# Kernel tuning notes

Measured on AMD Instinct MI355X. Metric: run time of the kernel, lower is better.

The kernel has to match this reference:

```python
import jax, jax.numpy as jnp
import numpy as np

N_NODES = 50000
N_EDGES = 640000
IN_F, H1, H2, H3, N_CLS = 128, 128, 128, 128, 40


def setup_inputs() -> dict:
    key = jax.random.key(0)
    ks = jax.random.split(key, 16)
    def lin(k, i, o):
        bound = 1.0 / np.sqrt(i)
        kw, kb = jax.random.split(k)
        W = jax.random.uniform(kw, (i, o), jnp.float32, -bound, bound)
        b = jax.random.uniform(kb, (o,), jnp.float32, -bound, bound)
        return W, b
    Wr, br = lin(ks[0], IN_F, H3)
    W1, b1 = lin(ks[1], IN_F, H1)
    W2, b2 = lin(ks[2], H1, H2)
    W3, b3 = lin(ks[3], H2, H3)
    Wop, bop = lin(ks[4], H3, N_CLS)
    x = jax.random.normal(ks[5], (N_NODES, IN_F), jnp.float32)
    src = jax.random.randint(ks[6], (N_EDGES,), 0, N_NODES, jnp.int64)
    dst = jax.random.randint(ks[7], (N_EDGES,), 0, N_NODES, jnp.int64)
    edge_weight = jax.random.uniform(ks[8], (N_EDGES,), jnp.float32)
    return {"x": x, "src": src, "dst": dst, "edge_weight": edge_weight,
            "Wr": Wr, "br": br, "W1": W1, "b1": b1, "W2": W2, "b2": b2,
            "W3": W3, "b3": b3, "Wop": Wop, "bop": bop}


def _gconv(x, src, dst, ew, W, b, n_nodes):
    # gather neighbor features, scale by edge weight, scatter-sum to dst, linear
    msg = x[src] * ew[:, None]                      # [E, d_in]
    agg = jax.ops.segment_sum(msg, dst, num_segments=n_nodes)  # [N, d_in]
    return agg @ W + b


def reference(x, src, dst, edge_weight, Wr, br, W1, b1, W2, b2, W3, b3, Wop, bop):
    n = x.shape[0]
    res = x @ Wr + br
    h = jax.nn.relu(_gconv(x, src, dst, edge_weight, W1, b1, n))
    h = jax.nn.relu(_gconv(h, src, dst, edge_weight, W2, b2, n))
    h = _gconv(h, src, dst, edge_weight, W3, b3, n)
    h = jax.nn.relu(h + res)
    return h @ Wop + bop
```

## Files before the change

### kernel.cpp

```cpp
#include <hip/hip_runtime.h>
#include <hip/hip_fp16.h>
#include <stdint.h>


#define NF 128

typedef unsigned short u16;
typedef unsigned int u32;
typedef __attribute__((ext_vector_type(8))) short short8;
typedef __attribute__((ext_vector_type(4))) float f32x4;

__device__ __forceinline__ float bf2f(u16 v) {
    union { unsigned u; float f; } x; x.u = (unsigned)v << 16; return x.f;
}
__device__ __forceinline__ u16 f2bf(float f) {
    union { float f; unsigned u; } x; x.f = f;
    unsigned r = (x.u + 0x7FFFu + ((x.u >> 16) & 1u)) >> 16;
    return (u16)r;
}

__global__ __launch_bounds__(256) void prep_all(
    const int* __restrict__ dst, int* __restrict__ counts, int* __restrict__ rank,
    int n_edges,
    const float* __restrict__ x, u16* __restrict__ xb, int n_feat,
    const float* __restrict__ Wr, const float* __restrict__ W1,
    const float* __restrict__ W2, const float* __restrict__ W3,
    const float* __restrict__ Wop, u16* __restrict__ Wt, u16* __restrict__ Wtop,
    int HB, int CB)
{
    int b = blockIdx.x;
    if (b < HB) {
        int e = b * 256 + threadIdx.x;
        if (e < n_edges) rank[e] = atomicAdd(&counts[dst[e]], 1);
    } else if (b < HB + CB) {
        int idx = ((b - HB) * 256 + threadIdx.x) * 4;
        if (idx < n_feat) {
            float4 v = *reinterpret_cast<const float4*>(x + idx);
            ushort4 o;
            o.x = f2bf(v.x); o.y = f2bf(v.y); o.z = f2bf(v.z); o.w = f2bf(v.w);
            *reinterpret_cast<ushort4*>(xb + idx) = o;
        }
    } else {
        int i = (b - HB - CB) * 256 + threadIdx.x;
        if (i < 4 * 16384) {
            int w = i >> 14, r = i & 16383;
            int nn = r >> 7, kk = r & 127;
            const float* W = (w == 0) ? Wr : (w == 1) ? W1 : (w == 2) ? W2 : W3;
            Wt[i] = f2bf(W[kk * NF + nn]);
        } else {
            int r = i - 4 * 16384;
            if (r < 48 * 128) {
                int nn = r >> 7, kk = r & 127;
                Wtop[r] = (nn < 40) ? f2bf(Wop[kk * 40 + nn]) : (u16)0;
            }
        }
    }
}

__global__ __launch_bounds__(256) void scan_pass1(
    const int* __restrict__ counts, int* __restrict__ bsums, int n)
{
    __shared__ int s[256];
    int i = blockIdx.x * 256 + threadIdx.x;
    int c = (i < n) ? counts[i] : 0;
    s[threadIdx.x] = (c + 3) & ~3;
    __syncthreads();
    for (int off = 128; off > 0; off >>= 1) {
        if (threadIdx.x < off) s[threadIdx.x] += s[threadIdx.x + off];
        __syncthreads();
    }
    if (threadIdx.x == 0) bsums[blockIdx.x] = s[0];
}

__global__ __launch_bounds__(256) void scan_pass23(
    int* __restrict__ rowptr, const int* __restrict__ bsums, int n, int G)
{
    __shared__ int s[256];
    int t = threadIdx.x;
    int bv = (t < G) ? bsums[t] : 0;
    s[t] = bv;
    __syncthreads();
    for (int off = 1; off < 256; off <<= 1) {
        int u = (t >= off) ? s[t - off] : 0;
        __syncthreads();
        s[t] += u;
        __syncthreads();
    }
    int blockoff = (blockIdx.x > 0) ? s[blockIdx.x - 1] : 0;
    int total = s[255];
    __syncthreads();

    int i = blockIdx.x * 256 + t;
    int c = (i < n) ? rowptr[i] : 0;
    int v = (c + 3) & ~3;
    s[t] = v;
    __syncthreads();
    for (int off = 1; off < 256; off <<= 1) {
        int u = (t >= off) ? s[t - off] : 0;
        __syncthreads();
        s[t] += u;
        __syncthreads();
    }
    int excl = s[t] - v + blockoff;
    if (i < n) rowptr[i] = excl;
    if (i == 0) rowptr[n] = total;
}

__global__ __launch_bounds__(256) void fill_packed(
    const int* __restrict__ src, const int* __restrict__ dst,
    const float* __restrict__ ew, const int* __restrict__ rowptr,
    const int* __restrict__ rank, u32* __restrict__ ppairs, int n_edges)
{
    int e = blockIdx.x * 256 + threadIdx.x;
    if (e >= n_edges) return;
    int pos = rowptr[dst[e]] + rank[e];
    ppairs[pos] = ((u32)src[e] << 16) |
                  (u32)__half_as_ushort(__float2half_rn(ew[e]));
}

__global__ __launch_bounds__(256) void agg_gather_b(
    const u16* __restrict__ xb, const int* __restrict__ rowptr,
    const u32* __restrict__ ppairs, u16* __restrict__ aggb, int n_nodes)
{
    int gid = blockIdx.x * 256 + threadIdx.x;
    int node = gid >> 4;
    if (node >= n_nodes) return;
    int f = (gid & 15) << 3;
    int e0 = rowptr[node];
    int e1 = rowptr[node + 1];
    const u16* xf = xb + f;

    float acc[8];
    #pragma unroll
    for (int j = 0; j < 8; j++) acc[j] = 0.f;

    int e = e0;
    for (; e + 8 <= e1; e += 8) {
        uint4 pa = *reinterpret_cast<const uint4*>(ppairs + e);
        uint4 pb = *reinterpret_cast<const uint4*>(ppairs + e + 4);
        u32 p[8] = {pa.x, pa.y, pa.z, pa.w, pb.x, pb.y, pb.z, pb.w};
        short8 v[8];
        #pragma unroll
        for (int k = 0; k < 8; k++)
            v[k] = *reinterpret_cast<const short8*>(xf + (size_t)(p[k] >> 16) * NF);
        #pragma unroll
        for (int k = 0; k < 8; k++) {
            float w = __half2float(__ushort_as_half((u16)(p[k] & 0xFFFFu)));
            #pragma unroll
            for (int j = 0; j < 8; j++)
                acc[j] = fmaf(bf2f((u16)v[k][j]), w, acc[j]);
        }
    }
    if (e < e1) {
        uint4 pa = *reinterpret_cast<const uint4*>(ppairs + e);
        u32 p[4] = {pa.x, pa.y, pa.z, pa.w};
        short8 v[4];
        #pragma unroll
        for (int k = 0; k < 4; k++)
            v[k] = *reinterpret_cast<const short8*>(xf + (size_t)(p[k] >> 16) * NF);
        #pragma unroll
        for (int k = 0; k < 4; k++) {
            float w = __half2float(__ushort_as_half((u16)(p[k] & 0xFFFFu)));
            #pragma unroll
            for (int j = 0; j < 8; j++)
                acc[j] = fmaf(bf2f((u16)v[k][j]), w, acc[j]);
        }
    }

    short8 o;
    #pragma unroll
    for (int j = 0; j < 8; j++) o[j] = (short)f2bf(acc[j]);
    *reinterpret_cast<short8*>(aggb + (size_t)node * NF + f) = o;
}

template<int RELU, int RES>
__global__ __launch_bounds__(256) void gemm_mfma128(
    const u16* __restrict__ A, const u16* __restrict__ Wt,
    const float* __restrict__ bias, const u16* __restrict__ resid,
    u16* __restrict__ out, int nrows)
{
    __shared__ u16 Bs[128 * 128];
    const int tid = threadIdx.x;
    #pragma unroll
    for (int i = 0; i < 8; i++) {
        int G = tid + i * 256;
        int row = G >> 4, g = G & 15, gs = g ^ (row & 7);
        *reinterpret_cast<short8*>(&Bs[row * NF + gs * 8]) =
            *reinterpret_cast<const short8*>(Wt + (size_t)G * 8);
    }
    __syncthreads();

    const int wave = tid >> 6, lane = tid & 63;
    const int lrow = lane & 15, lk = lane >> 4;

    #pragma unroll
    for (int sub = 0; sub < 2; ++sub) {
        const int row0 = blockIdx.x * 128 + sub * 64 + wave * 16;
        const int grow = row0 + lrow;

        short8 a[4];
        if (grow < nrows) {
            const u16* Ar = A + (size_t)grow * NF + lk * 8;
            #pragma unroll
            for (int t = 0; t < 4; t++)
                a[t] = *reinterpret_cast<const short8*>(Ar + t * 32);
        } else {
            #pragma unroll
            for (int t = 0; t < 4; t++)
                #pragma unroll
                for (int j = 0; j < 8; j++) a[t][j] = 0;
        }

        f32x4 acc[8];
        #pragma unroll
        for (int c = 0; c < 8; c++) { acc[c][0]=0.f; acc[c][1]=0.f; acc[c][2]=0.f; acc[c][3]=0.f; }

        #pragma unroll
        for (int t = 0; t < 4; t++) {
            #pragma unroll
            for (int c = 0; c < 8; c++) {
                int col = c * 16 + lrow;
                int g = t * 4 + lk, gs = g ^ (col & 7);
                short8 b = *reinterpret_cast<const short8*>(&Bs[col * NF + gs * 8]);
                acc[c] = __builtin_amdgcn_mfma_f32_16x16x32_bf16(a[t], b, acc[c], 0, 0, 0);
            }
        }

        #pragma unroll
        for (int c = 0; c < 8; c++) {
            int col = c * 16 + lrow;
            float bv = bias[col];
            #pragma unroll
            for (int r = 0; r < 4; r++) {
                int orow = row0 + lk * 4 + r;
                if (orow < nrows) {
                    float v = acc[c][r] + bv;
                    if (RES) v += bf2f(resid[(size_t)orow * NF + col]);
                    if (RELU) v = fmaxf(v, 0.f);
                    out[(size_t)orow * NF + col] = f2bf(v);
                }
            }
        }
    }
}

__global__ __launch_bounds__(256) void gemm_out40_mfma(
    const u16* __restrict__ H, const u16* __restrict__ Wtop,
    const float* __restrict__ bop, float* __restrict__ out, int nrows)
{
    __shared__ u16 Bs[48 * 128];
    const int tid = threadIdx.x;
    #pragma unroll
    for (int i = 0; i < 3; i++) {
        int G = tid + i * 256;
        int row = G >> 4, g = G & 15, gs = g ^ (row & 7);
        *reinterpret_cast<short8*>(&Bs[row * NF + gs * 8]) =
            *reinterpret_cast<const short8*>(Wtop + (size_t)G * 8);
    }
    __syncthreads();

    const int wave = tid >> 6, lane = tid & 63;
    const int lrow = lane & 15, lk = lane >> 4;

    #pragma unroll
    for (int sub = 0; sub < 2; ++sub) {
        const int row0 = blockIdx.x * 128 + sub * 64 + wave * 16;
        const int grow = row0 + lrow;

        short8 a[4];
        if (grow < nrows) {
            const u16* Hr = H + (size_t)grow * NF + lk * 8;
            #pragma unroll
            for (int t = 0; t < 4; t++)
                a[t] = *reinterpret_cast<const short8*>(Hr + t * 32);
        } else {
            #pragma unroll
            for (int t = 0; t < 4; t++)
                #pragma unroll
                for (int j = 0; j < 8; j++) a[t][j] = 0;
        }

        f32x4 acc[3];
        #pragma unroll
        for (int c = 0; c < 3; c++) { acc[c][0]=0.f; acc[c][1]=0.f; acc[c][2]=0.f; acc[c][3]=0.f; }

        #pragma unroll
        for (int t = 0; t < 4; t++) {
            #pragma unroll
            for (int c = 0; c < 3; c++) {
                int col = c * 16 + lrow;
                int g = t * 4 + lk, gs = g ^ (col & 7);
                short8 b = *reinterpret_cast<const short8*>(&Bs[col * NF + gs * 8]);
                acc[c] = __builtin_amdgcn_mfma_f32_16x16x32_bf16(a[t], b, acc[c], 0, 0, 0);
            }
        }

        #pragma unroll
        for (int c = 0; c < 3; c++) {
            int col = c * 16 + lrow;
            if (col < 40) {
                float bv = bop[col];
                #pragma unroll
                for (int r = 0; r < 4; r++) {
                    int orow = row0 + lk * 4 + r;
                    if (orow < nrows)
                        out[(size_t)orow * 40 + col] = acc[c][r] + bv;
                }
            }
        }
    }
}


extern "C" void kernel_launch(void* const* d_in, const int* in_sizes, int n_in,
                              void* d_out, int out_size, void* d_ws, size_t ws_size,
                              hipStream_t stream)
{
    const float* x   = (const float*)d_in[0];
    const int*   src = (const int*)d_in[1];
    const int*   dst = (const int*)d_in[2];
    const float* ew  = (const float*)d_in[3];
    const float* Wr  = (const float*)d_in[4];
    const float* br  = (const float*)d_in[5];
    const float* W1  = (const float*)d_in[6];
    const float* b1  = (const float*)d_in[7];
    const float* W2  = (const float*)d_in[8];
    const float* b2  = (const float*)d_in[9];
    const float* W3  = (const float*)d_in[10];
    const float* b3  = (const float*)d_in[11];
    const float* Wop = (const float*)d_in[12];
    const float* bop = (const float*)d_in[13];
    float* out = (float*)d_out;

    const int n_nodes = in_sizes[0] / NF;
    const int n_edges = in_sizes[1];
    const size_t feat = (size_t)n_nodes * NF;
    const int padded_cap = n_edges + 3 * n_nodes + 8;

    u16* xb   = (u16*)d_ws;
    u16* hb   = xb + feat;
    u16* aggb = hb + feat;
    u16* resb = aggb + feat;
    u16* Wt   = resb + feat;
    u16* Wtop = Wt + 4 * 16384;
    int* rowptr = (int*)(Wtop + 48 * 128);
    const int G1 = (n_nodes + 255) / 256;
    int* bsums  = rowptr + (n_nodes + 1);
    int* rank   = bsums + (G1 + 1);
    u32* ppairs = (u32*)(((uintptr_t)(rank + n_edges) + 15) & ~(uintptr_t)15);

    const int HB = (n_edges + 255) / 256;
    const int CB = ((int)feat / 4 + 255) / 256;
    const int PB = (4 * 16384 + 48 * 128 + 255) / 256;
    const int gemm_grid = (n_nodes + 127) / 128;
    const int agg_grid  = (n_nodes * 16 + 255) / 256;

    hipMemsetAsync(rowptr, 0, (size_t)(n_nodes + 1) * sizeof(int), stream);
    hipMemsetAsync(ppairs, 0, (size_t)padded_cap * sizeof(u32), stream);
    prep_all<<<HB + CB + PB, 256, 0, stream>>>(
        dst, rowptr, rank, n_edges, x, xb, (int)feat,
        Wr, W1, W2, W3, Wop, Wt, Wtop, HB, CB);
    scan_pass1<<<G1, 256, 0, stream>>>(rowptr, bsums, n_nodes);
    scan_pass23<<<G1, 256, 0, stream>>>(rowptr, bsums, n_nodes, G1);
    fill_packed<<<HB, 256, 0, stream>>>(src, dst, ew, rowptr, rank, ppairs, n_edges);

    gemm_mfma128<0, 0><<<gemm_grid, 256, 0, stream>>>(xb, Wt, br, nullptr, resb, n_nodes);

    agg_gather_b<<<agg_grid, 256, 0, stream>>>(xb, rowptr, ppairs, aggb, n_nodes);
    gemm_mfma128<1, 0><<<gemm_grid, 256, 0, stream>>>(aggb, Wt + 16384, b1, nullptr, hb, n_nodes);

    agg_gather_b<<<agg_grid, 256, 0, stream>>>(hb, rowptr, ppairs, aggb, n_nodes);
    gemm_mfma128<1, 0><<<gemm_grid, 256, 0, stream>>>(aggb, Wt + 2 * 16384, b2, nullptr, hb, n_nodes);

    agg_gather_b<<<agg_grid, 256, 0, stream>>>(hb, rowptr, ppairs, aggb, n_nodes);
    gemm_mfma128<1, 1><<<gemm_grid, 256, 0, stream>>>(aggb, Wt + 3 * 16384, b3, resb, hb, n_nodes);

    gemm_out40_mfma<<<gemm_grid, 256, 0, stream>>>(hb, Wtop, bop, out, n_nodes);
}
```

Before: 199.2 us.

## Fuse gather-aggregation with per-layer GEMM and final projection into one kernel

Each GNN layer now runs a single kernel: a block of 16 nodes gathers neighbor features into shared memory, then multiplies by the layer weight with MFMA and applies bias, ReLU and residual. The final layer also does the 40-class output projection in shared memory, so the aggb round trip and the separate output GEMM disappear. The residual GEMM is shrunk to 64 rows per block, and its A loads now overlap the weight staging. In exchange, weights are read straight from global/L2 with no LDS staging, and the 16-node blocks reload the weight matrix for every block.

```diff
diff --git a/kernel.cpp b/kernel.cpp
--- a/kernel.cpp
+++ b/kernel.cpp
@@ -118,66 +118,151 @@
                   (u32)__half_as_ushort(__float2half_rn(ew[e]));
 }
 
-__global__ __launch_bounds__(256) void agg_gather_b(
-    const u16* __restrict__ xb, const int* __restrict__ rowptr,
-    const u32* __restrict__ ppairs, u16* __restrict__ aggb, int n_nodes)
-{
-    int gid = blockIdx.x * 256 + threadIdx.x;
-    int node = gid >> 4;
-    if (node >= n_nodes) return;
-    int f = (gid & 15) << 3;
-    int e0 = rowptr[node];
-    int e1 = rowptr[node + 1];
-    const u16* xf = xb + f;
-
-    float acc[8];
-    #pragma unroll
-    for (int j = 0; j < 8; j++) acc[j] = 0.f;
-
-    int e = e0;
-    for (; e + 8 <= e1; e += 8) {
-        uint4 pa = *reinterpret_cast<const uint4*>(ppairs + e);
-        uint4 pb = *reinterpret_cast<const uint4*>(ppairs + e + 4);
-        u32 p[8] = {pa.x, pa.y, pa.z, pa.w, pb.x, pb.y, pb.z, pb.w};
-        short8 v[8];
-        #pragma unroll
-        for (int k = 0; k < 8; k++)
-            v[k] = *reinterpret_cast<const short8*>(xf + (size_t)(p[k] >> 16) * NF);
-        #pragma unroll
-        for (int k = 0; k < 8; k++) {
-            float w = __half2float(__ushort_as_half((u16)(p[k] & 0xFFFFu)));
+template<int RES, int PROJ>
+__global__ __launch_bounds__(256) void layer_gg(
+    const u16* __restrict__ X, const int* __restrict__ rowptr,
+    const u32* __restrict__ ppairs, const u16* __restrict__ Wt,
+    const float* __restrict__ bias, const u16* __restrict__ resid,
+    const u16* __restrict__ Wtop, const float* __restrict__ bop,
+    u16* __restrict__ hout, float* __restrict__ out, int n_nodes)
+{
+    __shared__ u16 As[16 * 128];
+    __shared__ u16 Hs[16 * 128];
+
+    const int tid = threadIdx.x;
+    const int node0 = blockIdx.x * 16;
+
+    {
+        const int nl = tid >> 4;
+        const int fl = tid & 15;
+        const int node = node0 + nl;
+        float acc[8];
+        #pragma unroll
+        for (int j = 0; j < 8; j++) acc[j] = 0.f;
+
+        if (node < n_nodes) {
+            const u16* xf = X + fl * 8;
+            int e0 = rowptr[node];
+            int e1 = rowptr[node + 1];
+            int e = e0;
+            for (; e + 8 <= e1; e += 8) {
+                uint4 pa = *reinterpret_cast<const uint4*>(ppairs + e);
+                uint4 pb = *reinterpret_cast<const uint4*>(ppairs + e + 4);
+                u32 p[8] = {pa.x, pa.y, pa.z, pa.w, pb.x, pb.y, pb.z, pb.w};
+                short8 v[8];
+                #pragma unroll
+                for (int k = 0; k < 8; k++)
+                    v[k] = *reinterpret_cast<const short8*>(xf + (size_t)(p[k] >> 16) * NF);
+                #pragma unroll
+                for (int k = 0; k < 8; k++) {
+                    float w = __half2float(__ushort_as_half((u16)(p[k] & 0xFFFFu)));
+                    #pragma unroll
+                    for (int j = 0; j < 8; j++)
+                        acc[j] = fmaf(bf2f((u16)v[k][j]), w, acc[j]);
+                }
+            }
+            if (e < e1) {
+                uint4 pa = *reinterpret_cast<const uint4*>(ppairs + e);
+                u32 p[4] = {pa.x, pa.y, pa.z, pa.w};
+                short8 v[4];
+                #pragma unroll
+                for (int k = 0; k < 4; k++)
+                    v[k] = *reinterpret_cast<const short8*>(xf + (size_t)(p[k] >> 16) * NF);
+                #pragma unroll
+                for (int k = 0; k < 4; k++) {
+                    float w = __half2float(__ushort_as_half((u16)(p[k] & 0xFFFFu)));
+                    #pragma unroll
+                    for (int j = 0; j < 8; j++)
+                        acc[j] = fmaf(bf2f((u16)v[k][j]), w, acc[j]);
+                }
+            }
+        }
+        short8 o;
+        #pragma unroll
+        for (int j = 0; j < 8; j++) o[j] = (short)f2bf(acc[j]);
+        int gs = fl ^ (nl & 7);
+        *reinterpret_cast<short8*>(&As[nl * NF + gs * 8]) = o;
+    }
+    __syncthreads();
+
+    const int wave = tid >> 6, lane = tid & 63;
+    const int lrow = lane & 15, lk = lane >> 4;
+
+    short8 a[4];
+    #pragma unroll
+    for (int t = 0; t < 4; t++) {
+        int g = t * 4 + lk, gs = g ^ (lrow & 7);
+        a[t] = *reinterpret_cast<const short8*>(&As[lrow * NF + gs * 8]);
+    }
+
+    f32x4 acc2[2];
+    #pragma unroll
+    for (int ct = 0; ct < 2; ct++) { acc2[ct][0]=0.f; acc2[ct][1]=0.f; acc2[ct][2]=0.f; acc2[ct][3]=0.f; }
+
+    #pragma unroll
+    for (int t = 0; t < 4; t++) {
+        #pragma unroll
+        for (int ct = 0; ct < 2; ct++) {
+            int col = wave * 32 + ct * 16 + lrow;
+            short8 b = *reinterpret_cast<const short8*>(Wt + (size_t)col * NF + (t * 4 + lk) * 8);
+            acc2[ct] = __builtin_amdgcn_mfma_f32_16x16x32_bf16(a[t], b, acc2[ct], 0, 0, 0);
+        }
+    }
+
+    #pragma unroll
+    for (int ct = 0; ct < 2; ct++) {
+        int col = wave * 32 + ct * 16 + lrow;
+        float bv = bias[col];
+        #pragma unroll
+        for (int r = 0; r < 4; r++) {
+            int row = lk * 4 + r;
+            int node = node0 + row;
+            if (node < n_nodes) {
+                float v = acc2[ct][r] + bv;
+                if (RES) v += bf2f(resid[(size_t)node * NF + col]);
+                v = fmaxf(v, 0.f);
+                if (!PROJ) {
+                    hout[(size_t)node * NF + col] = f2bf(v);
+                } else {
+                    Hs[row * NF + (((col >> 3) ^ (row & 7)) << 3) + (col & 7)] = f2bf(v);
+                }
+            }
+        }
+    }
+
+    if (PROJ) {
+        __syncthreads();
+        if (wave < 3) {
+            short8 pa[4];
             #pragma unroll
-            for (int j = 0; j < 8; j++)
-                acc[j] = fmaf(bf2f((u16)v[k][j]), w, acc[j]);
-        }
-    }
-    if (e < e1) {
-        uint4 pa = *reinterpret_cast<const uint4*>(ppairs + e);
-        u32 p[4] = {pa.x, pa.y, pa.z, pa.w};
-        short8 v[4];
-        #pragma unroll
-        for (int k = 0; k < 4; k++)
-            v[k] = *reinterpret_cast<const short8*>(xf + (size_t)(p[k] >> 16) * NF);
-        #pragma unroll
-        for (int k = 0; k < 4; k++) {
-            float w = __half2float(__ushort_as_half((u16)(p[k] & 0xFFFFu)));
+            for (int t = 0; t < 4; t++) {
+                int g = t * 4 + lk, gs = g ^ (lrow & 7);
+                pa[t] = *reinterpret_cast<const short8*>(&Hs[lrow * NF + gs * 8]);
+            }
+            f32x4 pacc;
+            pacc[0]=0.f; pacc[1]=0.f; pacc[2]=0.f; pacc[3]=0.f;
+            int col = wave * 16 + lrow;
             #pragma unroll
-            for (int j = 0; j < 8; j++)
-                acc[j] = fmaf(bf2f((u16)v[k][j]), w, acc[j]);
-        }
-    }
-
-    short8 o;
-    #pragma unroll
-    for (int j = 0; j < 8; j++) o[j] = (short)f2bf(acc[j]);
-    *reinterpret_cast<short8*>(aggb + (size_t)node * NF + f) = o;
-}
-
-template<int RELU, int RES>
-__global__ __launch_bounds__(256) void gemm_mfma128(
+            for (int t = 0; t < 4; t++) {
+                short8 b = *reinterpret_cast<const short8*>(Wtop + (size_t)col * NF + (t * 4 + lk) * 8);
+                pacc = __builtin_amdgcn_mfma_f32_16x16x32_bf16(pa[t], b, pacc, 0, 0, 0);
+            }
+            if (col < 40) {
+                float bv = bop[col];
+                #pragma unroll
+                for (int r = 0; r < 4; r++) {
+                    int node = node0 + lk * 4 + r;
+                    if (node < n_nodes)
+                        out[(size_t)node * 40 + col] = pacc[r] + bv;
+                }
+            }
+        }
+    }
+}
+
+__global__ __launch_bounds__(256) void gemm_mfma_res(
     const u16* __restrict__ A, const u16* __restrict__ Wt,
-    const float* __restrict__ bias, const u16* __restrict__ resid,
-    u16* __restrict__ out, int nrows)
+    const float* __restrict__ bias, u16* __restrict__ out, int nrows)
 {
     __shared__ u16 Bs[128 * 128];
     const int tid = threadIdx.x;
@@ -188,125 +273,50 @@
         *reinterpret_cast<short8*>(&Bs[row * NF + gs * 8]) =
             *reinterpret_cast<const short8*>(Wt + (size_t)G * 8);
     }
-    __syncthreads();
 
     const int wave = tid >> 6, lane = tid & 63;
     const int lrow = lane & 15, lk = lane >> 4;
-
-    #pragma unroll
-    for (int sub = 0; sub < 2; ++sub) {
-        const int row0 = blockIdx.x * 128 + sub * 64 + wave * 16;
-        const int grow = row0 + lrow;
-
-        short8 a[4];
-        if (grow < nrows) {
-            const u16* Ar = A + (size_t)grow * NF + lk * 8;
+    const int row0 = blockIdx.x * 64 + wave * 16;
+    const int grow = row0 + lrow;
+
+    short8 a[4];
+    if (grow < nrows) {
+        const u16* Ar = A + (size_t)grow * NF + lk * 8;
+        #pragma unroll
+        for (int t = 0; t < 4; t++)
+            a[t] = *reinterpret_cast<const short8*>(Ar + t * 32);
+    } else {
+        #pragma unroll
+        for (int t = 0; t < 4; t++)
             #pragma unroll
-            for (int t = 0; t < 4; t++)
-                a[t] = *reinterpret_cast<const short8*>(Ar + t * 32);
-        } else {
-            #pragma unroll
-            for (int t = 0; t < 4; t++)
-                #pragma unroll
-                for (int j = 0; j < 8; j++) a[t][j] = 0;
-        }
-
-        f32x4 acc[8];
-        #pragma unroll
-        for (int c = 0; c < 8; c++) { acc[c][0]=0.f; acc[c][1]=0.f; acc[c][2]=0.f; acc[c][3]=0.f; }
-
-        #pragma unroll
-        for (int t = 0; t < 4; t++) {
-            #pragma unroll
-            for (int c = 0; c < 8; c++) {
-                int col = c * 16 + lrow;
-                int g = t * 4 + lk, gs = g ^ (col & 7);
-                short8 b = *reinterpret_cast<const short8*>(&Bs[col * NF + gs * 8]);
-                acc[c] = __builtin_amdgcn_mfma_f32_16x16x32_bf16(a[t], b, acc[c], 0, 0, 0);
-            }
-        }
-
+            for (int j = 0; j < 8; j++) a[t][j] = 0;
+    }
+    __syncthreads();
+
+    f32x4 acc[8];
+    #pragma unroll
+    for (int c = 0; c < 8; c++) { acc[c][0]=0.f; acc[c][1]=0.f; acc[c][2]=0.f; acc[c][3]=0.f; }
+
+    #pragma unroll
+    for (int t = 0; t < 4; t++) {
         #pragma unroll
         for (int c = 0; c < 8; c++) {
             int col = c * 16 + lrow;
-            float bv = bias[col];
-            #pragma unroll
-            for (int r = 0; r < 4; r++) {
-                int orow = row0 + lk * 4 + r;
-                if (orow < nrows) {
-                    float v = acc[c][r] + bv;
-                    if (RES) v += bf2f(resid[(size_t)orow * NF + col]);
-                    if (RELU) v = fmaxf(v, 0.f);
-                    out[(size_t)orow * NF + col] = f2bf(v);
-                }
-            }
-        }
-    }
-}
-
-__global__ __launch_bounds__(256) void gemm_out40_mfma(
-    const u16* __restrict__ H, const u16* __restrict__ Wtop,
-    const float* __restrict__ bop, float* __restrict__ out, int nrows)
-{
-    __shared__ u16 Bs[48 * 128];
-    const int tid = threadIdx.x;
-    #pragma unroll
-    for (int i = 0; i < 3; i++) {
-        int G = tid + i * 256;
-        int row = G >> 4, g = G & 15, gs = g ^ (row & 7);
-        *reinterpret_cast<short8*>(&Bs[row * NF + gs * 8]) =
-            *reinterpret_cast<const short8*>(Wtop + (size_t)G * 8);
-    }
-    __syncthreads();
-
-    const int wave = tid >> 6, lane = tid & 63;
-    const int lrow = lane & 15, lk = lane >> 4;
-
-    #pragma unroll
-    for (int sub = 0; sub < 2; ++sub) {
-        const int row0 = blockIdx.x * 128 + sub * 64 + wave * 16;
-        const int grow = row0 + lrow;
-
-        short8 a[4];
-        if (grow < nrows) {
-            const u16* Hr = H + (size_t)grow * NF + lk * 8;
-            #pragma unroll
-            for (int t = 0; t < 4; t++)
-                a[t] = *reinterpret_cast<const short8*>(Hr + t * 32);
-        } else {
-            #pragma unroll
-            for (int t = 0; t < 4; t++)
-                #pragma unroll
-                for (int j = 0; j < 8; j++) a[t][j] = 0;
-        }
-
-        f32x4 acc[3];
-        #pragma unroll
-        for (int c = 0; c < 3; c++) { acc[c][0]=0.f; acc[c][1]=0.f; acc[c][2]=0.f; acc[c][3]=0.f; }
-
-        #pragma unroll
-        for (int t = 0; t < 4; t++) {
-            #pragma unroll
-            for (int c = 0; c < 3; c++) {
-                int col = c * 16 + lrow;
-                int g = t * 4 + lk, gs = g ^ (col & 7);
-                short8 b = *reinterpret_cast<const short8*>(&Bs[col * NF + gs * 8]);
-                acc[c] = __builtin_amdgcn_mfma_f32_16x16x32_bf16(a[t], b, acc[c], 0, 0, 0);
-            }
-        }
-
-        #pragma unroll
-        for (int c = 0; c < 3; c++) {
-            int col = c * 16 + lrow;
-            if (col < 40) {
-                float bv = bop[col];
-                #pragma unroll
-                for (int r = 0; r < 4; r++) {
-                    int orow = row0 + lk * 4 + r;
-                    if (orow < nrows)
-                        out[(size_t)orow * 40 + col] = acc[c][r] + bv;
-                }
-            }
+            int g = t * 4 + lk, gs = g ^ (col & 7);
+            short8 b = *reinterpret_cast<const short8*>(&Bs[col * NF + gs * 8]);
+            acc[c] = __builtin_amdgcn_mfma_f32_16x16x32_bf16(a[t], b, acc[c], 0, 0, 0);
+        }
+    }
+
+    #pragma unroll
+    for (int c = 0; c < 8; c++) {
+        int col = c * 16 + lrow;
+        float bv = bias[col];
+        #pragma unroll
+        for (int r = 0; r < 4; r++) {
+            int orow = row0 + lk * 4 + r;
+            if (orow < nrows)
+                out[(size_t)orow * NF + col] = f2bf(acc[c][r] + bv);
         }
     }
 }
@@ -338,9 +348,9 @@
     const int padded_cap = n_edges + 3 * n_nodes + 8;
 
     u16* xb   = (u16*)d_ws;
-    u16* hb   = xb + feat;
-    u16* aggb = hb + feat;
-    u16* resb = aggb + feat;
+    u16* h1b  = xb + feat;
+    u16* h2b  = h1b + feat;
+    u16* resb = h2b + feat;
     u16* Wt   = resb + feat;
     u16* Wtop = Wt + 4 * 16384;
     int* rowptr = (int*)(Wtop + 48 * 128);
@@ -352,8 +362,8 @@
     const int HB = (n_edges + 255) / 256;
     const int CB = ((int)feat / 4 + 255) / 256;
     const int PB = (4 * 16384 + 48 * 128 + 255) / 256;
-    const int gemm_grid = (n_nodes + 127) / 128;
-    const int agg_grid  = (n_nodes * 16 + 255) / 256;
+    const int res_grid   = (n_nodes + 63) / 64;
+    const int layer_grid = (n_nodes + 15) / 16;
 
     hipMemsetAsync(rowptr, 0, (size_t)(n_nodes + 1) * sizeof(int), stream);
     hipMemsetAsync(ppairs, 0, (size_t)padded_cap * sizeof(u32), stream);
@@ -364,16 +374,15 @@
     scan_pass23<<<G1, 256, 0, stream>>>(rowptr, bsums, n_nodes, G1);
     fill_packed<<<HB, 256, 0, stream>>>(src, dst, ew, rowptr, rank, ppairs, n_edges);
 
-    gemm_mfma128<0, 0><<<gemm_grid, 256, 0, stream>>>(xb, Wt, br, nullptr, resb, n_nodes);
-
-    agg_gather_b<<<agg_grid, 256, 0, stream>>>(xb, rowptr, ppairs, aggb, n_nodes);
-    gemm_mfma128<1, 0><<<gemm_grid, 256, 0, stream>>>(aggb, Wt + 16384, b1, nullptr, hb, n_nodes);
-
-    agg_gather_b<<<agg_grid, 256, 0, stream>>>(hb, rowptr, ppairs, aggb, n_nodes);
-    gemm_mfma128<1, 0><<<gemm_grid, 256, 0, stream>>>(aggb, Wt + 2 * 16384, b2, nullptr, hb, n_nodes);
-
-    agg_gather_b<<<agg_grid, 256, 0, stream>>>(hb, rowptr, ppairs, aggb, n_nodes);
-    gemm_mfma128<1, 1><<<gemm_grid, 256, 0, stream>>>(aggb, Wt + 3 * 16384, b3, resb, hb, n_nodes);
-
-    gemm_out40_mfma<<<gemm_grid, 256, 0, stream>>>(hb, Wtop, bop, out, n_nodes);
-}
+    gemm_mfma_res<<<res_grid, 256, 0, stream>>>(xb, Wt, br, resb, n_nodes);
+
+    layer_gg<0, 0><<<layer_grid, 256, 0, stream>>>(
+        xb, rowptr, ppairs, Wt + 16384, b1, nullptr, nullptr, nullptr,
+        h1b, nullptr, n_nodes);
+    layer_gg<0, 0><<<layer_grid, 256, 0, stream>>>(
+        h1b, rowptr, ppairs, Wt + 2 * 16384, b2, nullptr, nullptr, nullptr,
+        h2b, nullptr, n_nodes);
+    layer_gg<1, 1><<<layer_grid, 256, 0, stream>>>(
+        h2b, rowptr, ppairs, Wt + 3 * 16384, b3, resb, Wtop, bop,
+        nullptr, out, n_nodes);
+}
```

Result: faster. 191.1 us (-4.1%).

## Split gather into XCD-mapped feature slices and shrink GEMM row tiles

Applied to the files above, without the earlier changes.

The gather kernel now gives each block 64 nodes and one 32-feature slice. The slice is chosen from the block index modulo 8, so blocks running on the same pair of XCDs all touch the same quarter of the feature columns. That working set should fit in each XCD's L2 and reduce random-row misses to HBM. The mapping has 8 blocks per node group but only 4 slices, so every slice is computed and written twice, doubling gather compute and stores. Separately, the GEMM kernels now process 64 rows per block instead of 128, and issue the A-tile global loads before the barrier so they overlap with filling the weight tile in shared memory. This doubles the number of weight-tile loads.

```diff
diff --git a/kernel.cpp b/kernel.cpp
--- a/kernel.cpp
+++ b/kernel.cpp
@@ -118,18 +118,20 @@
                   (u32)__half_as_ushort(__float2half_rn(ew[e]));
 }
 
-__global__ __launch_bounds__(256) void agg_gather_b(
-    const u16* __restrict__ xb, const int* __restrict__ rowptr,
+__global__ __launch_bounds__(256) void gather_slice(
+    const u16* __restrict__ X, const int* __restrict__ rowptr,
     const u32* __restrict__ ppairs, u16* __restrict__ aggb, int n_nodes)
 {
-    int gid = blockIdx.x * 256 + threadIdx.x;
-    int node = gid >> 4;
+    const int b = blockIdx.x;
+    const int slice = (b & 7) >> 1;
+    const int t = threadIdx.x;
+    const int node = (b >> 3) * 64 + (t >> 2);
     if (node >= n_nodes) return;
-    int f = (gid & 15) << 3;
+    const int fo = slice * 32 + (t & 3) * 8;
+    const u16* xf = X + fo;
+
     int e0 = rowptr[node];
     int e1 = rowptr[node + 1];
-    const u16* xf = xb + f;
-
     float acc[8];
     #pragma unroll
     for (int j = 0; j < 8; j++) acc[j] = 0.f;
@@ -170,7 +172,7 @@
     short8 o;
     #pragma unroll
     for (int j = 0; j < 8; j++) o[j] = (short)f2bf(acc[j]);
-    *reinterpret_cast<short8*>(aggb + (size_t)node * NF + f) = o;
+    *reinterpret_cast<short8*>(aggb + (size_t)node * NF + fo) = o;
 }
 
 template<int RELU, int RES>
@@ -188,57 +190,53 @@
         *reinterpret_cast<short8*>(&Bs[row * NF + gs * 8]) =
             *reinterpret_cast<const short8*>(Wt + (size_t)G * 8);
     }
-    __syncthreads();
 
     const int wave = tid >> 6, lane = tid & 63;
     const int lrow = lane & 15, lk = lane >> 4;
-
-    #pragma unroll
-    for (int sub = 0; sub < 2; ++sub) {
-        const int row0 = blockIdx.x * 128 + sub * 64 + wave * 16;
-        const int grow = row0 + lrow;
-
-        short8 a[4];
-        if (grow < nrows) {
-            const u16* Ar = A + (size_t)grow * NF + lk * 8;
-            #pragma unroll
-            for (int t = 0; t < 4; t++)
-                a[t] = *reinterpret_cast<const short8*>(Ar + t * 32);
-        } else {
-            #pragma unroll
-            for (int t = 0; t < 4; t++)
-                #pragma unroll
-                for (int j = 0; j < 8; j++) a[t][j] = 0;
-        }
-
-        f32x4 acc[8];
-        #pragma unroll
-        for (int c = 0; c < 8; c++) { acc[c][0]=0.f; acc[c][1]=0.f; acc[c][2]=0.f; acc[c][3]=0.f; }
-
-        #pragma unroll
-        for (int t = 0; t < 4; t++) {
-            #pragma unroll
-            for (int c = 0; c < 8; c++) {
-                int col = c * 16 + lrow;
-                int g = t * 4 + lk, gs = g ^ (col & 7);
-                short8 b = *reinterpret_cast<const short8*>(&Bs[col * NF + gs * 8]);
-                acc[c] = __builtin_amdgcn_mfma_f32_16x16x32_bf16(a[t], b, acc[c], 0, 0, 0);
-            }
-        }
-
+    const int row0 = blockIdx.x * 64 + wave * 16;
+    const int grow = row0 + lrow;
+
+    short8 a[4];
+    if (grow < nrows) {
+        const u16* Ar = A + (size_t)grow * NF + lk * 8;
+        #pragma unroll
+        for (int t = 0; t < 4; t++)
+            a[t] = *reinterpret_cast<const short8*>(Ar + t * 32);
+    } else {
+        #pragma unroll
+        for (int t = 0; t < 4; t++)
+            #pragma unroll
+            for (int j = 0; j < 8; j++) a[t][j] = 0;
+    }
+    __syncthreads();
+
+    f32x4 acc[8];
+    #pragma unroll
+    for (int c = 0; c < 8; c++) { acc[c][0]=0.f; acc[c][1]=0.f; acc[c][2]=0.f; acc[c][3]=0.f; }
+
+    #pragma unroll
+    for (int t = 0; t < 4; t++) {
         #pragma unroll
         for (int c = 0; c < 8; c++) {
             int col = c * 16 + lrow;
-            float bv = bias[col];
-            #pragma unroll
-            for (int r = 0; r < 4; r++) {
-                int orow = row0 + lk * 4 + r;
-                if (orow < nrows) {
-                    float v = acc[c][r] + bv;
-                    if (RES) v += bf2f(resid[(size_t)orow * NF + col]);
-                    if (RELU) v = fmaxf(v, 0.f);
-                    out[(size_t)orow * NF + col] = f2bf(v);
-                }
+            int g = t * 4 + lk, gs = g ^ (col & 7);
+            short8 b = *reinterpret_cast<const short8*>(&Bs[col * NF + gs * 8]);
+            acc[c] = __builtin_amdgcn_mfma_f32_16x16x32_bf16(a[t], b, acc[c], 0, 0, 0);
+        }
+    }
+
+    #pragma unroll
+    for (int c = 0; c < 8; c++) {
+        int col = c * 16 + lrow;
+        float bv = bias[col];
+        #pragma unroll
+        for (int r = 0; r < 4; r++) {
+            int orow = row0 + lk * 4 + r;
+            if (orow < nrows) {
+                float v = acc[c][r] + bv;
+                if (RES) v += bf2f(resid[(size_t)orow * NF + col]);
+                if (RELU) v = fmaxf(v, 0.f);
+                out[(size_t)orow * NF + col] = f2bf(v);
             }
         }
     }
@@ -257,55 +255,51 @@
         *reinterpret_cast<short8*>(&Bs[row * NF + gs * 8]) =
             *reinterpret_cast<const short8*>(Wtop + (size_t)G * 8);
     }
-    __syncthreads();
 
     const int wave = tid >> 6, lane = tid & 63;
     const int lrow = lane & 15, lk = lane >> 4;
-
-    #pragma unroll
-    for (int sub = 0; sub < 2; ++sub) {
-        const int row0 = blockIdx.x * 128 + sub * 64 + wave * 16;
-        const int grow = row0 + lrow;
-
-        short8 a[4];
-        if (grow < nrows) {
-            const u16* Hr = H + (size_t)grow * NF + lk * 8;
-            #pragma unroll
-            for (int t = 0; t < 4; t++)
-                a[t] = *reinterpret_cast<const short8*>(Hr + t * 32);
-        } else {
-            #pragma unroll
-            for (int t = 0; t < 4; t++)
-                #pragma unroll
-                for (int j = 0; j < 8; j++) a[t][j] = 0;
-        }
-
-        f32x4 acc[3];
-        #pragma unroll
-        for (int c = 0; c < 3; c++) { acc[c][0]=0.f; acc[c][1]=0.f; acc[c][2]=0.f; acc[c][3]=0.f; }
-
-        #pragma unroll
-        for (int t = 0; t < 4; t++) {
-            #pragma unroll
-            for (int c = 0; c < 3; c++) {
-                int col = c * 16 + lrow;
-                int g = t * 4 + lk, gs = g ^ (col & 7);
-                short8 b = *reinterpret_cast<const short8*>(&Bs[col * NF + gs * 8]);
-                acc[c] = __builtin_amdgcn_mfma_f32_16x16x32_bf16(a[t], b, acc[c], 0, 0, 0);
-            }
-        }
-
+    const int row0 = blockIdx.x * 64 + wave * 16;
+    const int grow = row0 + lrow;
+
+    short8 a[4];
+    if (grow < nrows) {
+        const u16* Hr = H + (size_t)grow * NF + lk * 8;
+        #pragma unroll
+        for (int t = 0; t < 4; t++)
+            a[t] = *reinterpret_cast<const short8*>(Hr + t * 32);
+    } else {
+        #pragma unroll
+        for (int t = 0; t < 4; t++)
+            #pragma unroll
+            for (int j = 0; j < 8; j++) a[t][j] = 0;
+    }
+    __syncthreads();
+
+    f32x4 acc[3];
+    #pragma unroll
+    for (int c = 0; c < 3; c++) { acc[c][0]=0.f; acc[c][1]=0.f; acc[c][2]=0.f; acc[c][3]=0.f; }
+
+    #pragma unroll
+    for (int t = 0; t < 4; t++) {
         #pragma unroll
         for (int c = 0; c < 3; c++) {
             int col = c * 16 + lrow;
-            if (col < 40) {
-                float bv = bop[col];
-                #pragma unroll
-                for (int r = 0; r < 4; r++) {
-                    int orow = row0 + lk * 4 + r;
-                    if (orow < nrows)
-                        out[(size_t)orow * 40 + col] = acc[c][r] + bv;
-                }
+            int g = t * 4 + lk, gs = g ^ (col & 7);
+            short8 b = *reinterpret_cast<const short8*>(&Bs[col * NF + gs * 8]);
+            acc[c] = __builtin_amdgcn_mfma_f32_16x16x32_bf16(a[t], b, acc[c], 0, 0, 0);
+        }
+    }
+
+    #pragma unroll
+    for (int c = 0; c < 3; c++) {
+        int col = c * 16 + lrow;
+        if (col < 40) {
+            float bv = bop[col];
+            #pragma unroll
+            for (int r = 0; r < 4; r++) {
+                int orow = row0 + lk * 4 + r;
+                if (orow < nrows)
+                    out[(size_t)orow * 40 + col] = acc[c][r] + bv;
             }
         }
     }
@@ -352,8 +346,8 @@
     const int HB = (n_edges + 255) / 256;
     const int CB = ((int)feat / 4 + 255) / 256;
     const int PB = (4 * 16384 + 48 * 128 + 255) / 256;
-    const int gemm_grid = (n_nodes + 127) / 128;
-    const int agg_grid  = (n_nodes * 16 + 255) / 256;
+    const int gemm_grid   = (n_nodes + 63) / 64;
+    const int gather_grid = ((n_nodes + 63) / 64) * 8;
 
     hipMemsetAsync(rowptr, 0, (size_t)(n_nodes + 1) * sizeof(int), stream);
     hipMemsetAsync(ppairs, 0, (size_t)padded_cap * sizeof(u32), stream);
@@ -366,13 +360,13 @@
 
     gemm_mfma128<0, 0><<<gemm_grid, 256, 0, stream>>>(xb, Wt, br, nullptr, resb, n_nodes);
 
-    agg_gather_b<<<agg_grid, 256, 0, stream>>>(xb, rowptr, ppairs, aggb, n_nodes);
+    gather_slice<<<gather_grid, 256, 0, stream>>>(xb, rowptr, ppairs, aggb, n_nodes);
     gemm_mfma128<1, 0><<<gemm_grid, 256, 0, stream>>>(aggb, Wt + 16384, b1, nullptr, hb, n_nodes);
 
-    agg_gather_b<<<agg_grid, 256, 0, stream>>>(hb, rowptr, ppairs, aggb, n_nodes);
+    gather_slice<<<gather_grid, 256, 0, stream>>>(hb, rowptr, ppairs, aggb, n_nodes);
     gemm_mfma128<1, 0><<<gemm_grid, 256, 0, stream>>>(aggb, Wt + 2 * 16384, b2, nullptr, hb, n_nodes);
 
-    agg_gather_b<<<agg_grid, 256, 0, stream>>>(hb, rowptr, ppairs, aggb, n_nodes);
+    gather_slice<<<gather_grid, 256, 0, stream>>>(hb, rowptr, ppairs, aggb, n_nodes);
     gemm_mfma128<1, 1><<<gemm_grid, 256, 0, stream>>>(aggb, Wt + 3 * 16384, b3, resb, hb, n_nodes);
 
     gemm_out40_mfma<<<gemm_grid, 256, 0, stream>>>(hb, Wtop, bop, out, n_nodes);
```

Measured after the change: 294.5 us. 1.48x slower.
